# Performance work log

Hardware: AMD Instinct MI355X
Metric: run time of the kernel (lower is better)

Reference implementation:

```python
import jax, jax.numpy as jnp
import numpy as np

LN_EPS = 1e-5

def _layernorm(x):
    # LayerNorm over last dim, no affine (elementwise_affine=False)
    mu = jnp.mean(x, axis=-1, keepdims=True)
    var = jnp.var(x, axis=-1, keepdims=True)
    return (x - mu) * jax.lax.rsqrt(var + LN_EPS)

def setup_inputs() -> dict:
    key = jax.random.key(0)
    k1, k2, k3 = jax.random.split(key, 3)
    B, L, D = 2, 4096, 1024
    x = jax.random.normal(k1, (B, L, D), dtype=jnp.float32)
    W_qkv = jax.random.normal(k2, (3 * D, D), dtype=jnp.float32) * 0.02
    W_o = jax.random.normal(k3, (D, D), dtype=jnp.float32) * 0.02
    log_gamma = jnp.zeros((16,), dtype=jnp.float32)
    return {"x": x, "W_qkv": W_qkv, "W_o": W_o, "log_gamma": log_gamma}

def reference(x, W_qkv, W_o, log_gamma):
    B, L, D = x.shape
    H = log_gamma.shape[0]
    dk = D // H
    qkv = (x @ W_qkv.T).reshape(B, L, 3, H, dk)
    q, k, v = qkv[:, :, 0], qkv[:, :, 1], qkv[:, :, 2]  # [B,L,H,dk]
    k = _layernorm(k)
    gamma = jax.nn.sigmoid(log_gamma).reshape(1, H, 1, 1)  # per-head scalar decay
    # time-major for scan: [L,B,H,dk]
    qT = jnp.transpose(q, (1, 0, 2, 3))
    kT = jnp.transpose(k, (1, 0, 2, 3))
    vT = jnp.transpose(v, (1, 0, 2, 3))

    def step(S, qkv_t):
        q_t, k_t, v_t = qkv_t  # each [B,H,dk]
        # S(t) = gamma*S(t-1) + v_t (x) k_t ; shape [B,H,dk(d),dk(e)]
        S = gamma * S + v_t[..., :, None] * k_t[..., None, :]
        y_t = jnp.einsum('bhde,bhe->bhd', S, q_t)
        return S, y_t

    S0 = jnp.zeros((B, H, dk, dk), dtype=x.dtype)
    _, ys = jax.lax.scan(step, S0, (qT, kT, vT))  # ys: [L,B,H,dk]
    y = jnp.transpose(ys, (1, 0, 2, 3)).reshape(B, L, D)
    return y @ W_o.T
```

## Files before the change

### kernel.cpp

```cpp
#include <hip/hip_runtime.h>
#include <cstddef>

#define NB 2
#define NL 4096
#define ND 1024
#define NH 16
#define DKH 64
#define CK 64
#define NCH (NL / CK)
#define NM (NB * NL)
#define KD 1024

typedef __attribute__((ext_vector_type(8))) short bf16x8;
typedef __attribute__((ext_vector_type(4))) float f32x4;

__device__ __forceinline__ float dsigmoid(float x) { return 1.0f / (1.0f + __expf(-x)); }
__device__ __forceinline__ float bf2f(unsigned short u) { return __uint_as_float((unsigned)u << 16); }
__device__ __forceinline__ unsigned short f2bf(float f) {
    unsigned u = __float_as_uint(f);
    u = (u + 0x7fffu + ((u >> 16) & 1u)) >> 16;
    return (unsigned short)u;
}
__device__ __forceinline__ int swz(int row, int col) { return row * 64 + (col ^ ((row & 7) << 3)); }

__device__ __forceinline__ void gload16(const void* g, void* l) {
    __builtin_amdgcn_global_load_lds(
        (const __attribute__((address_space(1))) unsigned int*)g,
        (__attribute__((address_space(3))) unsigned int*)l, 16, 0, 0);
}

__global__ __launch_bounds__(256)
void k_cast_all(const float* __restrict__ x, const float* __restrict__ Wq,
                const float* __restrict__ Wo, unsigned short* __restrict__ xb,
                unsigned short* __restrict__ Wqb, unsigned short* __restrict__ Wob)
{
    const int N1 = NB * NL * ND / 4;
    const int N2 = 3 * ND * ND / 4;
    const int N3 = ND * ND / 4;
    const int total = N1 + N2 + N3;
    int i = blockIdx.x * 256 + threadIdx.x;
    const int stride = gridDim.x * 256;
    for (; i < total; i += stride) {
        const float4* src;
        ushort4* dst;
        int j;
        if (i < N1)            { src = (const float4*)x;  dst = (ushort4*)xb;  j = i; }
        else if (i < N1 + N2)  { src = (const float4*)Wq; dst = (ushort4*)Wqb; j = i - N1; }
        else                   { src = (const float4*)Wo; dst = (ushort4*)Wob; j = i - N1 - N2; }
        float4 v = src[j];
        ushort4 o;
        o.x = f2bf(v.x); o.y = f2bf(v.y); o.z = f2bf(v.z); o.w = f2bf(v.w);
        dst[j] = o;
    }
}

__global__ __launch_bounds__(256)
void k_gemm_qkv_bf16(const unsigned short* __restrict__ A, const unsigned short* __restrict__ Bm,
                     unsigned short* __restrict__ Qb, unsigned short* __restrict__ Kb,
                     unsigned short* __restrict__ Vb)
{
    __shared__ short As[128 * 64];
    __shared__ short Bs[128 * 64];
    const int tid = threadIdx.x;
    const int w = tid >> 6, lane = tid & 63;
    const int wr = w >> 1, wc = w & 1;
    const int lr = lane & 15, lk = lane >> 4;

    const int nbx = gridDim.x;
    const int nwg = nbx * gridDim.y;
    const int bid = blockIdx.y * nbx + blockIdx.x;
    const int sb  = (bid & 7) * (nwg >> 3) + (bid >> 3);
    const int row0 = (sb / nbx) * 128, col0 = (sb % nbx) * 128;

    const int srow = tid >> 3;
    const int schk = (tid & 7) ^ (srow & 7);
    const unsigned short* gA = A + (size_t)(row0 + srow) * KD + schk * 8;
    const unsigned short* gB = Bm + (size_t)(col0 + srow) * KD + schk * 8;
    short* lA = As + (w * 8) * 64;
    short* lB = Bs + (w * 8) * 64;

    f32x4 acc[4][4];
#pragma unroll
    for (int m = 0; m < 4; ++m)
#pragma unroll
        for (int n = 0; n < 4; ++n) acc[m][n] = (f32x4){0.f, 0.f, 0.f, 0.f};

    int arow[4], brow[4];
#pragma unroll
    for (int m = 0; m < 4; ++m) arow[m] = (wr * 64 + m * 16 + lr) * 64;
#pragma unroll
    for (int n = 0; n < 4; ++n) brow[n] = (wc * 64 + n * 16 + lr) * 64;
    const int xr = lr & 7;
    const int coff0 = ((0 * 4 + lk) ^ xr) * 8;
    const int coff1 = ((1 * 4 + lk) ^ xr) * 8;

    for (int k0 = 0; k0 < KD; k0 += 64) {
#pragma unroll
        for (int i = 0; i < 4; ++i) gload16(gA + (size_t)(i * 32) * KD + k0, lA + i * 2048);
#pragma unroll
        for (int i = 0; i < 4; ++i) gload16(gB + (size_t)(i * 32) * KD + k0, lB + i * 2048);
        __syncthreads();
#pragma unroll
        for (int kk = 0; kk < 2; ++kk) {
            const int co = kk ? coff1 : coff0;
            bf16x8 a[4], b[4];
#pragma unroll
            for (int m = 0; m < 4; ++m) a[m] = *(const bf16x8*)(As + arow[m] + co);
#pragma unroll
            for (int n = 0; n < 4; ++n) b[n] = *(const bf16x8*)(Bs + brow[n] + co);
#pragma unroll
            for (int m = 0; m < 4; ++m)
#pragma unroll
                for (int n = 0; n < 4; ++n)
                    acc[m][n] = __builtin_amdgcn_mfma_f32_16x16x32_bf16(a[m], b[n], acc[m][n], 0, 0, 0);
        }
        __syncthreads();
    }

#pragma unroll
    for (int m = 0; m < 4; ++m) {
        const int mrow0 = row0 + wr * 64 + m * 16 + lk * 4;
#pragma unroll
        for (int n = 0; n < 4; ++n) {
            const int gcol = col0 + wc * 64 + n * 16 + lr;
            const int three = gcol >> 10;
            const int h = (gcol >> 6) & (NH - 1);
            const int d = gcol & (DKH - 1);
            unsigned short* dst = (three == 0) ? Qb : ((three == 1) ? Kb : Vb);
#pragma unroll
            for (int j = 0; j < 4; ++j) {
                const int mr = mrow0 + j;
                const int b = mr >> 12;
                const int t = mr & (NL - 1);
                dst[(((size_t)b * NH + h) * NL + t) * DKH + d] = f2bf(acc[m][n][j]);
            }
        }
    }
}

__global__ __launch_bounds__(256)
void k_gemm_out_bf16(const unsigned short* __restrict__ A, const unsigned short* __restrict__ Bm,
                     float* __restrict__ C)
{
    __shared__ short As[128 * 64];
    __shared__ short Bs[128 * 64];
    const int tid = threadIdx.x;
    const int w = tid >> 6, lane = tid & 63;
    const int wr = w >> 1, wc = w & 1;
    const int lr = lane & 15, lk = lane >> 4;

    const int nbx = gridDim.x;
    const int nwg = nbx * gridDim.y;
    const int bid = blockIdx.y * nbx + blockIdx.x;
    const int sb  = (bid & 7) * (nwg >> 3) + (bid >> 3);
    const int row0 = (sb / nbx) * 128, col0 = (sb % nbx) * 128;

    const int srow = tid >> 3;
    const int schk = (tid & 7) ^ (srow & 7);
    const unsigned short* gA = A + (size_t)(row0 + srow) * KD + schk * 8;
    const unsigned short* gB = Bm + (size_t)(col0 + srow) * KD + schk * 8;
    short* lA = As + (w * 8) * 64;
    short* lB = Bs + (w * 8) * 64;

    f32x4 acc[4][4];
#pragma unroll
    for (int m = 0; m < 4; ++m)
#pragma unroll
        for (int n = 0; n < 4; ++n) acc[m][n] = (f32x4){0.f, 0.f, 0.f, 0.f};

    int arow[4], brow[4];
#pragma unroll
    for (int m = 0; m < 4; ++m) arow[m] = (wr * 64 + m * 16 + lr) * 64;
#pragma unroll
    for (int n = 0; n < 4; ++n) brow[n] = (wc * 64 + n * 16 + lr) * 64;
    const int xr = lr & 7;
    const int coff0 = ((0 * 4 + lk) ^ xr) * 8;
    const int coff1 = ((1 * 4 + lk) ^ xr) * 8;

    for (int k0 = 0; k0 < KD; k0 += 64) {
#pragma unroll
        for (int i = 0; i < 4; ++i) gload16(gA + (size_t)(i * 32) * KD + k0, lA + i * 2048);
#pragma unroll
        for (int i = 0; i < 4; ++i) gload16(gB + (size_t)(i * 32) * KD + k0, lB + i * 2048);
        __syncthreads();
#pragma unroll
        for (int kk = 0; kk < 2; ++kk) {
            const int co = kk ? coff1 : coff0;
            bf16x8 a[4], b[4];
#pragma unroll
            for (int m = 0; m < 4; ++m) a[m] = *(const bf16x8*)(As + arow[m] + co);
#pragma unroll
            for (int n = 0; n < 4; ++n) b[n] = *(const bf16x8*)(Bs + brow[n] + co);
#pragma unroll
            for (int m = 0; m < 4; ++m)
#pragma unroll
                for (int n = 0; n < 4; ++n)
                    acc[m][n] = __builtin_amdgcn_mfma_f32_16x16x32_bf16(a[m], b[n], acc[m][n], 0, 0, 0);
        }
        __syncthreads();
    }

#pragma unroll
    for (int m = 0; m < 4; ++m) {
        const int mrow0 = row0 + wr * 64 + m * 16 + lk * 4;
#pragma unroll
        for (int n = 0; n < 4; ++n) {
            const int gcol = col0 + wc * 64 + n * 16 + lr;
#pragma unroll
            for (int j = 0; j < 4; ++j)
                C[(size_t)(mrow0 + j) * ND + gcol] = acc[m][n][j];
        }
    }
}

__global__ __launch_bounds__(256)
void k_chunk_state(const unsigned short* __restrict__ Kb, const unsigned short* __restrict__ Vb,
                   const float* __restrict__ lg, unsigned short* __restrict__ SL)
{
    __shared__ unsigned short Kt[64 * 64];
    __shared__ unsigned short Vt[64 * 64];
    __shared__ float red[64][8];
    const int blk = blockIdx.x;
    const int c   = blk & (NCH - 1);
    const int bh  = blk >> 6;
    const int h   = bh & (NH - 1);
    const float gamma = dsigmoid(lg[h]);
    const float l2g = log2f(gamma);
    const int tid = threadIdx.x;
    const unsigned short* Kc = Kb + ((size_t)bh * NL + c * CK) * DKH;
    const unsigned short* Vc = Vb + ((size_t)bh * NL + c * CK) * DKH;

    const int r  = tid & 63;
    const int w4 = tid >> 6;
    const int c0 = w4 * 8;
    bf16x8 k8a = *(const bf16x8*)(Kc + (size_t)r * DKH + c0);
    bf16x8 k8b = *(const bf16x8*)(Kc + (size_t)r * DKH + c0 + 32);
    bf16x8 v8a = *(const bf16x8*)(Vc + (size_t)r * DKH + c0);
    bf16x8 v8b = *(const bf16x8*)(Vc + (size_t)r * DKH + c0 + 32);
    float sum = 0.f, sq = 0.f;
#pragma unroll
    for (int j = 0; j < 8; ++j) {
        float xa = bf2f((unsigned short)k8a[j]); sum += xa; sq += xa * xa;
        float xb = bf2f((unsigned short)k8b[j]); sum += xb; sq += xb * xb;
    }
    red[r][w4] = sum; red[r][w4 + 4] = sq;
    __syncthreads();
    float s  = red[r][0] + red[r][1] + red[r][2] + red[r][3];
    float qq = red[r][4] + red[r][5] + red[r][6] + red[r][7];
    float mu = s * (1.0f / 64.0f);
    float rstd = rsqrtf(qq * (1.0f / 64.0f) - mu * mu + 1e-5f);
    float wgt = exp2f((float)(CK - 1 - r) * l2g);
#pragma unroll
    for (int j = 0; j < 8; ++j) {
        Kt[swz(c0 + j, r)]      = f2bf((bf2f((unsigned short)k8a[j]) - mu) * rstd);
        Kt[swz(c0 + 32 + j, r)] = f2bf((bf2f((unsigned short)k8b[j]) - mu) * rstd);
        Vt[swz(c0 + j, r)]      = f2bf(bf2f((unsigned short)v8a[j]) * wgt);
        Vt[swz(c0 + 32 + j, r)] = f2bf(bf2f((unsigned short)v8b[j]) * wgt);
    }
    __syncthreads();

    const int w = tid >> 6, lane = tid & 63;
    const int wr = w >> 1, wc = w & 1;
    const int lr = lane & 15, lk = lane >> 4;
    f32x4 acc[2][2];
#pragma unroll
    for (int m = 0; m < 2; ++m)
#pragma unroll
        for (int n = 0; n < 2; ++n) acc[m][n] = (f32x4){0.f, 0.f, 0.f, 0.f};
#pragma unroll
    for (int kk = 0; kk < 2; ++kk) {
        const int so = kk * 32 + lk * 8;
        bf16x8 a[2], b[2];
#pragma unroll
        for (int m = 0; m < 2; ++m) a[m] = *(const bf16x8*)&Vt[swz(wr * 32 + m * 16 + lr, so)];
#pragma unroll
        for (int n = 0; n < 2; ++n) b[n] = *(const bf16x8*)&Kt[swz(wc * 32 + n * 16 + lr, so)];
#pragma unroll
        for (int m = 0; m < 2; ++m)
#pragma unroll
            for (int n = 0; n < 2; ++n)
                acc[m][n] = __builtin_amdgcn_mfma_f32_16x16x32_bf16(a[m], b[n], acc[m][n], 0, 0, 0);
    }

    unsigned short* out = SL + (size_t)blk * (DKH * DKH);
#pragma unroll
    for (int m = 0; m < 2; ++m)
#pragma unroll
        for (int n = 0; n < 2; ++n)
#pragma unroll
            for (int j = 0; j < 4; ++j) {
                int d = wr * 32 + m * 16 + lk * 4 + j;
                int e = wc * 32 + n * 16 + lr;
                out[d * DKH + e] = f2bf(acc[m][n][j]);
            }
}

__global__ __launch_bounds__(64)
void k_scan(const unsigned short* __restrict__ SL, const float* __restrict__ lg,
            unsigned short* __restrict__ SS)
{
    const int bh = blockIdx.x;
    const int qt = blockIdx.y;
    const int h  = bh & (NH - 1);
    const float gamma = dsigmoid(lg[h]);
    const float dc = __powf(gamma, (float)CK);
    const size_t base = (size_t)bh * NCH * (DKH * DKH) + qt * 256 + threadIdx.x * 4;
    float s0 = 0.f, s1 = 0.f, s2 = 0.f, s3 = 0.f;
    for (int c = 0; c < NCH; ++c) {
        const size_t off = base + (size_t)c * (DKH * DKH);
        ushort4 l = *(const ushort4*)(SL + off);
        ushort4 o;
        o.x = f2bf(s0); o.y = f2bf(s1); o.z = f2bf(s2); o.w = f2bf(s3);
        *(ushort4*)(SS + off) = o;
        s0 = s0 * dc + bf2f(l.x); s1 = s1 * dc + bf2f(l.y);
        s2 = s2 * dc + bf2f(l.z); s3 = s3 * dc + bf2f(l.w);
    }
}

__global__ __launch_bounds__(256)
void k_chunk_out(const unsigned short* __restrict__ Qb, const unsigned short* __restrict__ Kb,
                 const unsigned short* __restrict__ Vb, const unsigned short* __restrict__ SS,
                 const float* __restrict__ lg, unsigned short* __restrict__ Y)
{
    __shared__ unsigned short Qs[64 * 64];
    __shared__ unsigned short Ks[64 * 64];
    __shared__ unsigned short Vt[64 * 64];
    __shared__ unsigned short Ss[64 * 64];
    __shared__ unsigned short Ps[64 * 64];
    __shared__ float red[64][8];
    const int blk = blockIdx.x;
    const int c   = blk & (NCH - 1);
    const int bh  = blk >> 6;
    const int h   = bh & (NH - 1);
    const int b   = bh >> 4;
    const float gamma = dsigmoid(lg[h]);
    const float l2g = log2f(gamma);
    const int tid = threadIdx.x;
    const unsigned short* Qc = Qb + ((size_t)bh * NL + c * CK) * DKH;
    const unsigned short* Kc = Kb + ((size_t)bh * NL + c * CK) * DKH;
    const unsigned short* Vc = Vb + ((size_t)bh * NL + c * CK) * DKH;
    const unsigned short* Sc = SS + (size_t)blk * (DKH * DKH);

    const int r  = tid & 63;
    const int w4 = tid >> 6;
    const int c0 = w4 * 8;
    bf16x8 q8a = *(const bf16x8*)(Qc + (size_t)r * DKH + c0);
    bf16x8 q8b = *(const bf16x8*)(Qc + (size_t)r * DKH + c0 + 32);
    bf16x8 k8a = *(const bf16x8*)(Kc + (size_t)r * DKH + c0);
    bf16x8 k8b = *(const bf16x8*)(Kc + (size_t)r * DKH + c0 + 32);
    bf16x8 v8a = *(const bf16x8*)(Vc + (size_t)r * DKH + c0);
    bf16x8 v8b = *(const bf16x8*)(Vc + (size_t)r * DKH + c0 + 32);
    bf16x8 s8a = *(const bf16x8*)(Sc + (size_t)r * DKH + c0);
    bf16x8 s8b = *(const bf16x8*)(Sc + (size_t)r * DKH + c0 + 32);
    float sum = 0.f, sq = 0.f;
#pragma unroll
    for (int j = 0; j < 8; ++j) {
        float xa = bf2f((unsigned short)k8a[j]); sum += xa; sq += xa * xa;
        float xb = bf2f((unsigned short)k8b[j]); sum += xb; sq += xb * xb;
    }
    red[r][w4] = sum; red[r][w4 + 4] = sq;
    __syncthreads();
    float sm = red[r][0] + red[r][1] + red[r][2] + red[r][3];
    float qq = red[r][4] + red[r][5] + red[r][6] + red[r][7];
    float mu = sm * (1.0f / 64.0f);
    float rstd = rsqrtf(qq * (1.0f / 64.0f) - mu * mu + 1e-5f);
    *(bf16x8*)&Qs[swz(r, c0)]      = q8a;
    *(bf16x8*)&Qs[swz(r, c0 + 32)] = q8b;
    *(bf16x8*)&Ss[swz(r, c0)]      = s8a;
    *(bf16x8*)&Ss[swz(r, c0 + 32)] = s8b;
#pragma unroll
    for (int j = 0; j < 8; ++j) {
        Ks[swz(r, c0 + j)]      = f2bf((bf2f((unsigned short)k8a[j]) - mu) * rstd);
        Ks[swz(r, c0 + 32 + j)] = f2bf((bf2f((unsigned short)k8b[j]) - mu) * rstd);
        Vt[swz(c0 + j, r)]      = (unsigned short)v8a[j];
        Vt[swz(c0 + 32 + j, r)] = (unsigned short)v8b[j];
    }
    __syncthreads();

    const int w = tid >> 6, lane = tid & 63;
    const int wr = w >> 1, wc = w & 1;
    const int lr = lane & 15, lk = lane >> 4;

    f32x4 accp[2][2];
#pragma unroll
    for (int m = 0; m < 2; ++m)
#pragma unroll
        for (int n = 0; n < 2; ++n) accp[m][n] = (f32x4){0.f, 0.f, 0.f, 0.f};
#pragma unroll
    for (int kk = 0; kk < 2; ++kk) {
        const int eo = kk * 32 + lk * 8;
        bf16x8 a[2], bfr[2];
#pragma unroll
        for (int m = 0; m < 2; ++m) a[m]   = *(const bf16x8*)&Qs[swz(wr * 32 + m * 16 + lr, eo)];
#pragma unroll
        for (int n = 0; n < 2; ++n) bfr[n] = *(const bf16x8*)&Ks[swz(wc * 32 + n * 16 + lr, eo)];
#pragma unroll
        for (int m = 0; m < 2; ++m)
#pragma unroll
            for (int n = 0; n < 2; ++n)
                accp[m][n] = __builtin_amdgcn_mfma_f32_16x16x32_bf16(a[m], bfr[n], accp[m][n], 0, 0, 0);
    }
#pragma unroll
    for (int m = 0; m < 2; ++m)
#pragma unroll
        for (int n = 0; n < 2; ++n)
#pragma unroll
            for (int j = 0; j < 4; ++j) {
                int t = wr * 32 + m * 16 + lk * 4 + j;
                int s = wc * 32 + n * 16 + lr;
                int dt = t - s;
                float v = (dt >= 0) ? accp[m][n][j] * exp2f((float)dt * l2g) : 0.0f;
                Ps[swz(t, s)] = f2bf(v);
            }
    __syncthreads();

    f32x4 accy[2][2], accz[2][2];
#pragma unroll
    for (int m = 0; m < 2; ++m)
#pragma unroll
        for (int n = 0; n < 2; ++n) {
            accy[m][n] = (f32x4){0.f, 0.f, 0.f, 0.f};
            accz[m][n] = (f32x4){0.f, 0.f, 0.f, 0.f};
        }
#pragma unroll
    for (int kk = 0; kk < 2; ++kk) {
        const int so = kk * 32 + lk * 8;
        bf16x8 pa[2], qa[2], vb[2], sb[2];
#pragma unroll
        for (int m = 0; m < 2; ++m) {
            pa[m] = *(const bf16x8*)&Ps[swz(wr * 32 + m * 16 + lr, so)];
            qa[m] = *(const bf16x8*)&Qs[swz(wr * 32 + m * 16 + lr, so)];
        }
#pragma unroll
        for (int n = 0; n < 2; ++n) {
            vb[n] = *(const bf16x8*)&Vt[swz(wc * 32 + n * 16 + lr, so)];
            sb[n] = *(const bf16x8*)&Ss[swz(wc * 32 + n * 16 + lr, so)];
        }
#pragma unroll
        for (int m = 0; m < 2; ++m)
#pragma unroll
            for (int n = 0; n < 2; ++n) {
                accy[m][n] = __builtin_amdgcn_mfma_f32_16x16x32_bf16(pa[m], vb[n], accy[m][n], 0, 0, 0);
                accz[m][n] = __builtin_amdgcn_mfma_f32_16x16x32_bf16(qa[m], sb[n], accz[m][n], 0, 0, 0);
            }
    }
    __syncthreads();

#pragma unroll
    for (int m = 0; m < 2; ++m)
#pragma unroll
        for (int n = 0; n < 2; ++n)
#pragma unroll
            for (int j = 0; j < 4; ++j) {
                int t = wr * 32 + m * 16 + lk * 4 + j;
                int d = wc * 32 + n * 16 + lr;
                float g = exp2f((float)(t + 1) * l2g);
                Ps[swz(t, d)] = f2bf(accy[m][n][j] + g * accz[m][n][j]);
            }
    __syncthreads();

#pragma unroll
    for (int i = 0; i < 2; ++i) {
        int f  = tid + i * 256;
        int rr = f >> 3;
        int ch = f & 7;
        bf16x8 val = *(const bf16x8*)&Ps[swz(rr, ch * 8)];
        unsigned short* p = Y + ((size_t)(b * NL + c * CK + rr)) * ND + h * DKH + ch * 8;
        *(bf16x8*)p = val;
    }
}

extern "C" void kernel_launch(void* const* d_in, const int* in_sizes, int n_in,
                              void* d_out, int out_size, void* d_ws, size_t ws_size,
                              hipStream_t stream)
{
    (void)in_sizes; (void)n_in; (void)out_size; (void)ws_size;
    const float* x  = (const float*)d_in[0];
    const float* Wq = (const float*)d_in[1];
    const float* Wo = (const float*)d_in[2];
    const float* lg = (const float*)d_in[3];
    float* out = (float*)d_out;

    const size_t SZ = (size_t)NB * NH * NL * DKH;
    unsigned short* xb  = (unsigned short*)d_ws;
    unsigned short* Wqb = xb + SZ;
    unsigned short* Wob = Wqb + (size_t)3 * ND * ND;
    unsigned short* Qb  = Wob + (size_t)ND * ND;
    unsigned short* Kb  = Qb + SZ;
    unsigned short* Vb  = Kb + SZ;
    unsigned short* SL  = Vb + SZ;
    unsigned short* SS  = SL + SZ;
    unsigned short* Ybb = SS + SZ;

    k_cast_all<<<2048, 256, 0, stream>>>(x, Wq, Wo, xb, Wqb, Wob);
    k_gemm_qkv_bf16<<<dim3(3 * ND / 128, NM / 128), 256, 0, stream>>>(xb, Wqb, Qb, Kb, Vb);
    k_chunk_state<<<dim3(NB * NH * NCH), 256, 0, stream>>>(Kb, Vb, lg, SL);
    k_scan<<<dim3(NB * NH, 16), 64, 0, stream>>>(SL, lg, SS);
    k_chunk_out<<<dim3(NB * NH * NCH), 256, 0, stream>>>(Qb, Kb, Vb, SS, lg, Ybb);
    k_gemm_out_bf16<<<dim3(ND / 128, NM / 128), 256, 0, stream>>>(Ybb, Wob, out);
}
```

Before: 135.3 us.

## Group four chunks per block and carry intra-group state in registers

State computation and the inter-chunk scan now work on groups of four 64-token chunks. Each block of the output kernel keeps the running state in MFMA accumulators and updates it chunk by chunk, so the scan covers 16 groups instead of 64 chunks and less state is written to and read from global memory. The price is a quarter as many blocks (512) in the state and output kernels, which lowers parallelism on the GPU, plus extra MFMA work and LDS traffic per chunk inside the output kernel. Next-chunk loads are double-buffered in registers to hide global latency.

```diff
diff --git a/kernel.cpp b/kernel.cpp
--- a/kernel.cpp
+++ b/kernel.cpp
@@ -8,6 +8,7 @@
 #define DKH 64
 #define CK 64
 #define NCH (NL / CK)
+#define NG 16
 #define NM (NB * NL)
 #define KD 1024
 
@@ -214,75 +215,99 @@
 }
 
 __global__ __launch_bounds__(256)
-void k_chunk_state(const unsigned short* __restrict__ Kb, const unsigned short* __restrict__ Vb,
-                   const float* __restrict__ lg, unsigned short* __restrict__ SL)
+void k_group_state(const unsigned short* __restrict__ Kb, const unsigned short* __restrict__ Vb,
+                   const float* __restrict__ lg, unsigned short* __restrict__ GL)
 {
     __shared__ unsigned short Kt[64 * 64];
     __shared__ unsigned short Vt[64 * 64];
     __shared__ float red[64][8];
     const int blk = blockIdx.x;
-    const int c   = blk & (NCH - 1);
-    const int bh  = blk >> 6;
+    const int g   = blk & (NG - 1);
+    const int bh  = blk >> 4;
     const int h   = bh & (NH - 1);
     const float gamma = dsigmoid(lg[h]);
-    const float l2g = log2f(gamma);
+    const float l2g  = log2f(gamma);
+    const float dc64 = exp2f(64.0f * l2g);
     const int tid = threadIdx.x;
-    const unsigned short* Kc = Kb + ((size_t)bh * NL + c * CK) * DKH;
-    const unsigned short* Vc = Vb + ((size_t)bh * NL + c * CK) * DKH;
-
     const int r  = tid & 63;
     const int w4 = tid >> 6;
     const int c0 = w4 * 8;
-    bf16x8 k8a = *(const bf16x8*)(Kc + (size_t)r * DKH + c0);
-    bf16x8 k8b = *(const bf16x8*)(Kc + (size_t)r * DKH + c0 + 32);
-    bf16x8 v8a = *(const bf16x8*)(Vc + (size_t)r * DKH + c0);
-    bf16x8 v8b = *(const bf16x8*)(Vc + (size_t)r * DKH + c0 + 32);
-    float sum = 0.f, sq = 0.f;
-#pragma unroll
-    for (int j = 0; j < 8; ++j) {
-        float xa = bf2f((unsigned short)k8a[j]); sum += xa; sq += xa * xa;
-        float xb = bf2f((unsigned short)k8b[j]); sum += xb; sq += xb * xb;
-    }
-    red[r][w4] = sum; red[r][w4 + 4] = sq;
-    __syncthreads();
-    float s  = red[r][0] + red[r][1] + red[r][2] + red[r][3];
-    float qq = red[r][4] + red[r][5] + red[r][6] + red[r][7];
-    float mu = s * (1.0f / 64.0f);
-    float rstd = rsqrtf(qq * (1.0f / 64.0f) - mu * mu + 1e-5f);
-    float wgt = exp2f((float)(CK - 1 - r) * l2g);
-#pragma unroll
-    for (int j = 0; j < 8; ++j) {
-        Kt[swz(c0 + j, r)]      = f2bf((bf2f((unsigned short)k8a[j]) - mu) * rstd);
-        Kt[swz(c0 + 32 + j, r)] = f2bf((bf2f((unsigned short)k8b[j]) - mu) * rstd);
-        Vt[swz(c0 + j, r)]      = f2bf(bf2f((unsigned short)v8a[j]) * wgt);
-        Vt[swz(c0 + 32 + j, r)] = f2bf(bf2f((unsigned short)v8b[j]) * wgt);
-    }
-    __syncthreads();
-
     const int w = tid >> 6, lane = tid & 63;
     const int wr = w >> 1, wc = w & 1;
     const int lr = lane & 15, lk = lane >> 4;
+
     f32x4 acc[2][2];
 #pragma unroll
     for (int m = 0; m < 2; ++m)
 #pragma unroll
         for (int n = 0; n < 2; ++n) acc[m][n] = (f32x4){0.f, 0.f, 0.f, 0.f};
-#pragma unroll
-    for (int kk = 0; kk < 2; ++kk) {
-        const int so = kk * 32 + lk * 8;
-        bf16x8 a[2], b[2];
-#pragma unroll
-        for (int m = 0; m < 2; ++m) a[m] = *(const bf16x8*)&Vt[swz(wr * 32 + m * 16 + lr, so)];
-#pragma unroll
-        for (int n = 0; n < 2; ++n) b[n] = *(const bf16x8*)&Kt[swz(wc * 32 + n * 16 + lr, so)];
-#pragma unroll
-        for (int m = 0; m < 2; ++m)
-#pragma unroll
-            for (int n = 0; n < 2; ++n)
-                acc[m][n] = __builtin_amdgcn_mfma_f32_16x16x32_bf16(a[m], b[n], acc[m][n], 0, 0, 0);
-    }
-
-    unsigned short* out = SL + (size_t)blk * (DKH * DKH);
+
+    bf16x8 k8[2][2], v8[2][2];
+    {
+        const unsigned short* Kc = Kb + ((size_t)bh * NL + (g * 4) * CK) * DKH;
+        const unsigned short* Vc = Vb + ((size_t)bh * NL + (g * 4) * CK) * DKH;
+        k8[0][0] = *(const bf16x8*)(Kc + (size_t)r * DKH + c0);
+        k8[0][1] = *(const bf16x8*)(Kc + (size_t)r * DKH + c0 + 32);
+        v8[0][0] = *(const bf16x8*)(Vc + (size_t)r * DKH + c0);
+        v8[0][1] = *(const bf16x8*)(Vc + (size_t)r * DKH + c0 + 32);
+    }
+
+#pragma unroll
+    for (int ci = 0; ci < 4; ++ci) {
+        const int cb = ci & 1;
+        float sum = 0.f, sq = 0.f;
+#pragma unroll
+        for (int j = 0; j < 8; ++j) {
+            float xa = bf2f((unsigned short)k8[cb][0][j]); sum += xa; sq += xa * xa;
+            float xb = bf2f((unsigned short)k8[cb][1][j]); sum += xb; sq += xb * xb;
+        }
+        red[r][w4] = sum; red[r][w4 + 4] = sq;
+        __syncthreads();
+        float sm = red[r][0] + red[r][1] + red[r][2] + red[r][3];
+        float qq = red[r][4] + red[r][5] + red[r][6] + red[r][7];
+        float mu = sm * (1.0f / 64.0f);
+        float rstd = rsqrtf(qq * (1.0f / 64.0f) - mu * mu + 1e-5f);
+        float wgt = exp2f((float)(CK - 1 - r) * l2g);
+#pragma unroll
+        for (int j = 0; j < 8; ++j) {
+            Kt[swz(c0 + j, r)]      = f2bf((bf2f((unsigned short)k8[cb][0][j]) - mu) * rstd * wgt);
+            Kt[swz(c0 + 32 + j, r)] = f2bf((bf2f((unsigned short)k8[cb][1][j]) - mu) * rstd * wgt);
+            Vt[swz(c0 + j, r)]      = (unsigned short)v8[cb][0][j];
+            Vt[swz(c0 + 32 + j, r)] = (unsigned short)v8[cb][1][j];
+        }
+        if (ci < 3) {
+            const int c = g * 4 + ci + 1;
+            const unsigned short* Kc = Kb + ((size_t)bh * NL + c * CK) * DKH;
+            const unsigned short* Vc = Vb + ((size_t)bh * NL + c * CK) * DKH;
+            k8[cb ^ 1][0] = *(const bf16x8*)(Kc + (size_t)r * DKH + c0);
+            k8[cb ^ 1][1] = *(const bf16x8*)(Kc + (size_t)r * DKH + c0 + 32);
+            v8[cb ^ 1][0] = *(const bf16x8*)(Vc + (size_t)r * DKH + c0);
+            v8[cb ^ 1][1] = *(const bf16x8*)(Vc + (size_t)r * DKH + c0 + 32);
+        }
+        __syncthreads();
+        if (ci > 0) {
+#pragma unroll
+            for (int m = 0; m < 2; ++m)
+#pragma unroll
+                for (int n = 0; n < 2; ++n) acc[m][n] = acc[m][n] * dc64;
+        }
+#pragma unroll
+        for (int kk = 0; kk < 2; ++kk) {
+            const int so = kk * 32 + lk * 8;
+            bf16x8 a[2], b[2];
+#pragma unroll
+            for (int m = 0; m < 2; ++m) a[m] = *(const bf16x8*)&Vt[swz(wr * 32 + m * 16 + lr, so)];
+#pragma unroll
+            for (int n = 0; n < 2; ++n) b[n] = *(const bf16x8*)&Kt[swz(wc * 32 + n * 16 + lr, so)];
+#pragma unroll
+            for (int m = 0; m < 2; ++m)
+#pragma unroll
+                for (int n = 0; n < 2; ++n)
+                    acc[m][n] = __builtin_amdgcn_mfma_f32_16x16x32_bf16(a[m], b[n], acc[m][n], 0, 0, 0);
+        }
+    }
+
+    unsigned short* out = GL + (size_t)blk * (DKH * DKH);
 #pragma unroll
     for (int m = 0; m < 2; ++m)
 #pragma unroll
@@ -296,177 +321,224 @@
 }
 
 __global__ __launch_bounds__(64)
-void k_scan(const unsigned short* __restrict__ SL, const float* __restrict__ lg,
-            unsigned short* __restrict__ SS)
+void k_scan16(const unsigned short* __restrict__ GL, const float* __restrict__ lg,
+              unsigned short* __restrict__ GS)
 {
     const int bh = blockIdx.x;
     const int qt = blockIdx.y;
     const int h  = bh & (NH - 1);
     const float gamma = dsigmoid(lg[h]);
-    const float dc = __powf(gamma, (float)CK);
-    const size_t base = (size_t)bh * NCH * (DKH * DKH) + qt * 256 + threadIdx.x * 4;
+    const float dc = exp2f(256.0f * log2f(gamma));
+    const size_t base = (size_t)bh * NG * (DKH * DKH) + qt * 256 + threadIdx.x * 4;
     float s0 = 0.f, s1 = 0.f, s2 = 0.f, s3 = 0.f;
-    for (int c = 0; c < NCH; ++c) {
-        const size_t off = base + (size_t)c * (DKH * DKH);
-        ushort4 l = *(const ushort4*)(SL + off);
+    for (int g = 0; g < NG; ++g) {
+        const size_t off = base + (size_t)g * (DKH * DKH);
+        ushort4 l = *(const ushort4*)(GL + off);
         ushort4 o;
         o.x = f2bf(s0); o.y = f2bf(s1); o.z = f2bf(s2); o.w = f2bf(s3);
-        *(ushort4*)(SS + off) = o;
+        *(ushort4*)(GS + off) = o;
         s0 = s0 * dc + bf2f(l.x); s1 = s1 * dc + bf2f(l.y);
         s2 = s2 * dc + bf2f(l.z); s3 = s3 * dc + bf2f(l.w);
     }
 }
 
 __global__ __launch_bounds__(256)
-void k_chunk_out(const unsigned short* __restrict__ Qb, const unsigned short* __restrict__ Kb,
-                 const unsigned short* __restrict__ Vb, const unsigned short* __restrict__ SS,
-                 const float* __restrict__ lg, unsigned short* __restrict__ Y)
+void k_chunk_out4(const unsigned short* __restrict__ Qb, const unsigned short* __restrict__ Kb,
+                  const unsigned short* __restrict__ Vb, const unsigned short* __restrict__ GS,
+                  const float* __restrict__ lg, unsigned short* __restrict__ Y)
 {
     __shared__ unsigned short Qs[64 * 64];
     __shared__ unsigned short Ks[64 * 64];
+    __shared__ unsigned short Kwt[64 * 64];
     __shared__ unsigned short Vt[64 * 64];
-    __shared__ unsigned short Ss[64 * 64];
     __shared__ unsigned short Ps[64 * 64];
+    __shared__ unsigned short Sbf[64 * 64];
     __shared__ float red[64][8];
     const int blk = blockIdx.x;
-    const int c   = blk & (NCH - 1);
-    const int bh  = blk >> 6;
+    const int g   = blk & (NG - 1);
+    const int bh  = blk >> 4;
     const int h   = bh & (NH - 1);
     const int b   = bh >> 4;
     const float gamma = dsigmoid(lg[h]);
-    const float l2g = log2f(gamma);
+    const float l2g  = log2f(gamma);
+    const float dc64 = exp2f(64.0f * l2g);
     const int tid = threadIdx.x;
-    const unsigned short* Qc = Qb + ((size_t)bh * NL + c * CK) * DKH;
-    const unsigned short* Kc = Kb + ((size_t)bh * NL + c * CK) * DKH;
-    const unsigned short* Vc = Vb + ((size_t)bh * NL + c * CK) * DKH;
-    const unsigned short* Sc = SS + (size_t)blk * (DKH * DKH);
-
     const int r  = tid & 63;
     const int w4 = tid >> 6;
     const int c0 = w4 * 8;
-    bf16x8 q8a = *(const bf16x8*)(Qc + (size_t)r * DKH + c0);
-    bf16x8 q8b = *(const bf16x8*)(Qc + (size_t)r * DKH + c0 + 32);
-    bf16x8 k8a = *(const bf16x8*)(Kc + (size_t)r * DKH + c0);
-    bf16x8 k8b = *(const bf16x8*)(Kc + (size_t)r * DKH + c0 + 32);
-    bf16x8 v8a = *(const bf16x8*)(Vc + (size_t)r * DKH + c0);
-    bf16x8 v8b = *(const bf16x8*)(Vc + (size_t)r * DKH + c0 + 32);
-    bf16x8 s8a = *(const bf16x8*)(Sc + (size_t)r * DKH + c0);
-    bf16x8 s8b = *(const bf16x8*)(Sc + (size_t)r * DKH + c0 + 32);
-    float sum = 0.f, sq = 0.f;
-#pragma unroll
-    for (int j = 0; j < 8; ++j) {
-        float xa = bf2f((unsigned short)k8a[j]); sum += xa; sq += xa * xa;
-        float xb = bf2f((unsigned short)k8b[j]); sum += xb; sq += xb * xb;
-    }
-    red[r][w4] = sum; red[r][w4 + 4] = sq;
-    __syncthreads();
-    float sm = red[r][0] + red[r][1] + red[r][2] + red[r][3];
-    float qq = red[r][4] + red[r][5] + red[r][6] + red[r][7];
-    float mu = sm * (1.0f / 64.0f);
-    float rstd = rsqrtf(qq * (1.0f / 64.0f) - mu * mu + 1e-5f);
-    *(bf16x8*)&Qs[swz(r, c0)]      = q8a;
-    *(bf16x8*)&Qs[swz(r, c0 + 32)] = q8b;
-    *(bf16x8*)&Ss[swz(r, c0)]      = s8a;
-    *(bf16x8*)&Ss[swz(r, c0 + 32)] = s8b;
-#pragma unroll
-    for (int j = 0; j < 8; ++j) {
-        Ks[swz(r, c0 + j)]      = f2bf((bf2f((unsigned short)k8a[j]) - mu) * rstd);
-        Ks[swz(r, c0 + 32 + j)] = f2bf((bf2f((unsigned short)k8b[j]) - mu) * rstd);
-        Vt[swz(c0 + j, r)]      = (unsigned short)v8a[j];
-        Vt[swz(c0 + 32 + j, r)] = (unsigned short)v8b[j];
-    }
-    __syncthreads();
-
     const int w = tid >> 6, lane = tid & 63;
     const int wr = w >> 1, wc = w & 1;
     const int lr = lane & 15, lk = lane >> 4;
 
-    f32x4 accp[2][2];
+    {
+        const unsigned short* Gp = GS + (size_t)blk * (DKH * DKH);
+        *(bf16x8*)&Sbf[swz(r, c0)]      = *(const bf16x8*)(Gp + (size_t)r * DKH + c0);
+        *(bf16x8*)&Sbf[swz(r, c0 + 32)] = *(const bf16x8*)(Gp + (size_t)r * DKH + c0 + 32);
+    }
+    __syncthreads();
+    f32x4 S_acc[2][2];
 #pragma unroll
     for (int m = 0; m < 2; ++m)
 #pragma unroll
-        for (int n = 0; n < 2; ++n) accp[m][n] = (f32x4){0.f, 0.f, 0.f, 0.f};
-#pragma unroll
-    for (int kk = 0; kk < 2; ++kk) {
-        const int eo = kk * 32 + lk * 8;
-        bf16x8 a[2], bfr[2];
-#pragma unroll
-        for (int m = 0; m < 2; ++m) a[m]   = *(const bf16x8*)&Qs[swz(wr * 32 + m * 16 + lr, eo)];
-#pragma unroll
-        for (int n = 0; n < 2; ++n) bfr[n] = *(const bf16x8*)&Ks[swz(wc * 32 + n * 16 + lr, eo)];
+        for (int n = 0; n < 2; ++n)
+#pragma unroll
+            for (int j = 0; j < 4; ++j)
+                S_acc[m][n][j] = bf2f(Sbf[swz(wr * 32 + m * 16 + lk * 4 + j, wc * 32 + n * 16 + lr)]);
+
+    bf16x8 q8[2][2], k8[2][2], v8[2][2];
+    {
+        const size_t rowb = ((size_t)bh * NL + (g * 4) * CK + r) * DKH;
+        q8[0][0] = *(const bf16x8*)(Qb + rowb + c0);
+        q8[0][1] = *(const bf16x8*)(Qb + rowb + c0 + 32);
+        k8[0][0] = *(const bf16x8*)(Kb + rowb + c0);
+        k8[0][1] = *(const bf16x8*)(Kb + rowb + c0 + 32);
+        v8[0][0] = *(const bf16x8*)(Vb + rowb + c0);
+        v8[0][1] = *(const bf16x8*)(Vb + rowb + c0 + 32);
+    }
+
+#pragma unroll
+    for (int ci = 0; ci < 4; ++ci) {
+        const int cb = ci & 1;
+        const int c  = g * 4 + ci;
+        float sum = 0.f, sq = 0.f;
+#pragma unroll
+        for (int j = 0; j < 8; ++j) {
+            float xa = bf2f((unsigned short)k8[cb][0][j]); sum += xa; sq += xa * xa;
+            float xb = bf2f((unsigned short)k8[cb][1][j]); sum += xb; sq += xb * xb;
+        }
+        red[r][w4] = sum; red[r][w4 + 4] = sq;
+        __syncthreads();
+        float sm = red[r][0] + red[r][1] + red[r][2] + red[r][3];
+        float qq = red[r][4] + red[r][5] + red[r][6] + red[r][7];
+        float mu = sm * (1.0f / 64.0f);
+        float rstd = rsqrtf(qq * (1.0f / 64.0f) - mu * mu + 1e-5f);
+        float wgt = exp2f((float)(CK - 1 - r) * l2g);
+        *(bf16x8*)&Qs[swz(r, c0)]      = q8[cb][0];
+        *(bf16x8*)&Qs[swz(r, c0 + 32)] = q8[cb][1];
+#pragma unroll
+        for (int j = 0; j < 8; ++j) {
+            float ka = (bf2f((unsigned short)k8[cb][0][j]) - mu) * rstd;
+            float kb_ = (bf2f((unsigned short)k8[cb][1][j]) - mu) * rstd;
+            Ks[swz(r, c0 + j)]       = f2bf(ka);
+            Ks[swz(r, c0 + 32 + j)]  = f2bf(kb_);
+            Kwt[swz(c0 + j, r)]      = f2bf(ka * wgt);
+            Kwt[swz(c0 + 32 + j, r)] = f2bf(kb_ * wgt);
+            Vt[swz(c0 + j, r)]       = (unsigned short)v8[cb][0][j];
+            Vt[swz(c0 + 32 + j, r)]  = (unsigned short)v8[cb][1][j];
+        }
 #pragma unroll
         for (int m = 0; m < 2; ++m)
 #pragma unroll
             for (int n = 0; n < 2; ++n)
-                accp[m][n] = __builtin_amdgcn_mfma_f32_16x16x32_bf16(a[m], bfr[n], accp[m][n], 0, 0, 0);
-    }
-#pragma unroll
-    for (int m = 0; m < 2; ++m)
-#pragma unroll
-        for (int n = 0; n < 2; ++n)
-#pragma unroll
-            for (int j = 0; j < 4; ++j) {
-                int t = wr * 32 + m * 16 + lk * 4 + j;
-                int s = wc * 32 + n * 16 + lr;
-                int dt = t - s;
-                float v = (dt >= 0) ? accp[m][n][j] * exp2f((float)dt * l2g) : 0.0f;
-                Ps[swz(t, s)] = f2bf(v);
+#pragma unroll
+                for (int j = 0; j < 4; ++j)
+                    Sbf[swz(wr * 32 + m * 16 + lk * 4 + j, wc * 32 + n * 16 + lr)] =
+                        f2bf(S_acc[m][n][j]);
+        __syncthreads();
+
+        f32x4 accp[2][2];
+#pragma unroll
+        for (int m = 0; m < 2; ++m)
+#pragma unroll
+            for (int n = 0; n < 2; ++n) accp[m][n] = (f32x4){0.f, 0.f, 0.f, 0.f};
+#pragma unroll
+        for (int kk = 0; kk < 2; ++kk) {
+            const int eo = kk * 32 + lk * 8;
+            bf16x8 a[2], bfr[2];
+#pragma unroll
+            for (int m = 0; m < 2; ++m) a[m]   = *(const bf16x8*)&Qs[swz(wr * 32 + m * 16 + lr, eo)];
+#pragma unroll
+            for (int n = 0; n < 2; ++n) bfr[n] = *(const bf16x8*)&Ks[swz(wc * 32 + n * 16 + lr, eo)];
+#pragma unroll
+            for (int m = 0; m < 2; ++m)
+#pragma unroll
+                for (int n = 0; n < 2; ++n)
+                    accp[m][n] = __builtin_amdgcn_mfma_f32_16x16x32_bf16(a[m], bfr[n], accp[m][n], 0, 0, 0);
+        }
+#pragma unroll
+        for (int m = 0; m < 2; ++m)
+#pragma unroll
+            for (int n = 0; n < 2; ++n)
+#pragma unroll
+                for (int j = 0; j < 4; ++j) {
+                    int t = wr * 32 + m * 16 + lk * 4 + j;
+                    int s = wc * 32 + n * 16 + lr;
+                    int dt = t - s;
+                    float v = (dt >= 0) ? accp[m][n][j] * exp2f((float)dt * l2g) : 0.0f;
+                    Ps[swz(t, s)] = f2bf(v);
+                }
+        if (ci < 3) {
+            const size_t rowb = ((size_t)bh * NL + (c + 1) * CK + r) * DKH;
+            q8[cb ^ 1][0] = *(const bf16x8*)(Qb + rowb + c0);
+            q8[cb ^ 1][1] = *(const bf16x8*)(Qb + rowb + c0 + 32);
+            k8[cb ^ 1][0] = *(const bf16x8*)(Kb + rowb + c0);
+            k8[cb ^ 1][1] = *(const bf16x8*)(Kb + rowb + c0 + 32);
+            v8[cb ^ 1][0] = *(const bf16x8*)(Vb + rowb + c0);
+            v8[cb ^ 1][1] = *(const bf16x8*)(Vb + rowb + c0 + 32);
+        }
+        __syncthreads();
+
+#pragma unroll
+        for (int m = 0; m < 2; ++m)
+#pragma unroll
+            for (int n = 0; n < 2; ++n) S_acc[m][n] = S_acc[m][n] * dc64;
+        f32x4 accy[2][2], accz[2][2];
+#pragma unroll
+        for (int m = 0; m < 2; ++m)
+#pragma unroll
+            for (int n = 0; n < 2; ++n) {
+                accy[m][n] = (f32x4){0.f, 0.f, 0.f, 0.f};
+                accz[m][n] = (f32x4){0.f, 0.f, 0.f, 0.f};
             }
-    __syncthreads();
-
-    f32x4 accy[2][2], accz[2][2];
-#pragma unroll
-    for (int m = 0; m < 2; ++m)
-#pragma unroll
-        for (int n = 0; n < 2; ++n) {
-            accy[m][n] = (f32x4){0.f, 0.f, 0.f, 0.f};
-            accz[m][n] = (f32x4){0.f, 0.f, 0.f, 0.f};
-        }
-#pragma unroll
-    for (int kk = 0; kk < 2; ++kk) {
-        const int so = kk * 32 + lk * 8;
-        bf16x8 pa[2], qa[2], vb[2], sb[2];
-#pragma unroll
-        for (int m = 0; m < 2; ++m) {
-            pa[m] = *(const bf16x8*)&Ps[swz(wr * 32 + m * 16 + lr, so)];
-            qa[m] = *(const bf16x8*)&Qs[swz(wr * 32 + m * 16 + lr, so)];
-        }
-#pragma unroll
-        for (int n = 0; n < 2; ++n) {
-            vb[n] = *(const bf16x8*)&Vt[swz(wc * 32 + n * 16 + lr, so)];
-            sb[n] = *(const bf16x8*)&Ss[swz(wc * 32 + n * 16 + lr, so)];
-        }
+#pragma unroll
+        for (int kk = 0; kk < 2; ++kk) {
+            const int so = kk * 32 + lk * 8;
+            bf16x8 pa[2], qa[2], va[2], vb[2], sb[2], kb2[2];
+#pragma unroll
+            for (int m = 0; m < 2; ++m) {
+                pa[m] = *(const bf16x8*)&Ps[swz(wr * 32 + m * 16 + lr, so)];
+                qa[m] = *(const bf16x8*)&Qs[swz(wr * 32 + m * 16 + lr, so)];
+                va[m] = *(const bf16x8*)&Vt[swz(wr * 32 + m * 16 + lr, so)];
+            }
+#pragma unroll
+            for (int n = 0; n < 2; ++n) {
+                vb[n]  = *(const bf16x8*)&Vt[swz(wc * 32 + n * 16 + lr, so)];
+                sb[n]  = *(const bf16x8*)&Sbf[swz(wc * 32 + n * 16 + lr, so)];
+                kb2[n] = *(const bf16x8*)&Kwt[swz(wc * 32 + n * 16 + lr, so)];
+            }
+#pragma unroll
+            for (int m = 0; m < 2; ++m)
+#pragma unroll
+                for (int n = 0; n < 2; ++n) {
+                    accy[m][n]  = __builtin_amdgcn_mfma_f32_16x16x32_bf16(pa[m], vb[n],  accy[m][n], 0, 0, 0);
+                    accz[m][n]  = __builtin_amdgcn_mfma_f32_16x16x32_bf16(qa[m], sb[n],  accz[m][n], 0, 0, 0);
+                    S_acc[m][n] = __builtin_amdgcn_mfma_f32_16x16x32_bf16(va[m], kb2[n], S_acc[m][n], 0, 0, 0);
+                }
+        }
+        __syncthreads();
+
 #pragma unroll
         for (int m = 0; m < 2; ++m)
 #pragma unroll
-            for (int n = 0; n < 2; ++n) {
-                accy[m][n] = __builtin_amdgcn_mfma_f32_16x16x32_bf16(pa[m], vb[n], accy[m][n], 0, 0, 0);
-                accz[m][n] = __builtin_amdgcn_mfma_f32_16x16x32_bf16(qa[m], sb[n], accz[m][n], 0, 0, 0);
-            }
-    }
-    __syncthreads();
-
-#pragma unroll
-    for (int m = 0; m < 2; ++m)
-#pragma unroll
-        for (int n = 0; n < 2; ++n)
-#pragma unroll
-            for (int j = 0; j < 4; ++j) {
-                int t = wr * 32 + m * 16 + lk * 4 + j;
-                int d = wc * 32 + n * 16 + lr;
-                float g = exp2f((float)(t + 1) * l2g);
-                Ps[swz(t, d)] = f2bf(accy[m][n][j] + g * accz[m][n][j]);
-            }
-    __syncthreads();
-
-#pragma unroll
-    for (int i = 0; i < 2; ++i) {
-        int f  = tid + i * 256;
-        int rr = f >> 3;
-        int ch = f & 7;
-        bf16x8 val = *(const bf16x8*)&Ps[swz(rr, ch * 8)];
-        unsigned short* p = Y + ((size_t)(b * NL + c * CK + rr)) * ND + h * DKH + ch * 8;
-        *(bf16x8*)p = val;
+            for (int n = 0; n < 2; ++n)
+#pragma unroll
+                for (int j = 0; j < 4; ++j) {
+                    int t = wr * 32 + m * 16 + lk * 4 + j;
+                    int d = wc * 32 + n * 16 + lr;
+                    float ge = exp2f((float)(t + 1) * l2g);
+                    Ps[swz(t, d)] = f2bf(accy[m][n][j] + ge * accz[m][n][j]);
+                }
+        __syncthreads();
+
+#pragma unroll
+        for (int i = 0; i < 2; ++i) {
+            int f  = tid + i * 256;
+            int rr = f >> 3;
+            int ch = f & 7;
+            bf16x8 val = *(const bf16x8*)&Ps[swz(rr, ch * 8)];
+            unsigned short* p = Y + ((size_t)(b * NL + c * CK + rr)) * ND + h * DKH + ch * 8;
+            *(bf16x8*)p = val;
+        }
     }
 }
 
@@ -481,21 +553,22 @@
     const float* lg = (const float*)d_in[3];
     float* out = (float*)d_out;
 
-    const size_t SZ = (size_t)NB * NH * NL * DKH;
+    const size_t SZ  = (size_t)NB * NH * NL * DKH;
+    const size_t GSZ = (size_t)NB * NH * NG * DKH * DKH;
     unsigned short* xb  = (unsigned short*)d_ws;
     unsigned short* Wqb = xb + SZ;
     unsigned short* Wob = Wqb + (size_t)3 * ND * ND;
     unsigned short* Qb  = Wob + (size_t)ND * ND;
     unsigned short* Kb  = Qb + SZ;
     unsigned short* Vb  = Kb + SZ;
-    unsigned short* SL  = Vb + SZ;
-    unsigned short* SS  = SL + SZ;
-    unsigned short* Ybb = SS + SZ;
+    unsigned short* GL  = Vb + SZ;
+    unsigned short* GS  = GL + GSZ;
+    unsigned short* Ybb = GS + GSZ;
 
     k_cast_all<<<2048, 256, 0, stream>>>(x, Wq, Wo, xb, Wqb, Wob);
     k_gemm_qkv_bf16<<<dim3(3 * ND / 128, NM / 128), 256, 0, stream>>>(xb, Wqb, Qb, Kb, Vb);
-    k_chunk_state<<<dim3(NB * NH * NCH), 256, 0, stream>>>(Kb, Vb, lg, SL);
-    k_scan<<<dim3(NB * NH, 16), 64, 0, stream>>>(SL, lg, SS);
-    k_chunk_out<<<dim3(NB * NH * NCH), 256, 0, stream>>>(Qb, Kb, Vb, SS, lg, Ybb);
+    k_group_state<<<dim3(NB * NH * NG), 256, 0, stream>>>(Kb, Vb, lg, GL);
+    k_scan16<<<dim3(NB * NH, 16), 64, 0, stream>>>(GL, lg, GS);
+    k_chunk_out4<<<dim3(NB * NH * NG), 256, 0, stream>>>(Qb, Kb, Vb, GS, lg, Ybb);
     k_gemm_out_bf16<<<dim3(ND / 128, NM / 128), 256, 0, stream>>>(Ybb, Wob, out);
 }
```

After: 136.0 us. Within noise of the previous version (+0.5%).

## Fuse K layernorm into QKV GEMM epilogue and widen cast kernel stores

Applied to the files above, without the earlier changes.

The per-head layernorm of K moves into the QKV GEMM epilogue, using wave shuffles across the 64 columns each wave holds per head. This removes the duplicated LN reduction, shared-memory reduction array and extra barrier from both chunk kernels. In k_chunk_state the decay weight now scales K instead of V, which is mathematically equivalent. The cast kernel also handles 8 elements per thread with 16-byte stores. The cost is extra epilogue work in the GEMM blocks that produce K, and K is now rounded to bf16 after normalisation rather than before.

```diff
diff --git a/kernel.cpp b/kernel.cpp
--- a/kernel.cpp
+++ b/kernel.cpp
@@ -34,22 +34,26 @@
                 const float* __restrict__ Wo, unsigned short* __restrict__ xb,
                 unsigned short* __restrict__ Wqb, unsigned short* __restrict__ Wob)
 {
-    const int N1 = NB * NL * ND / 4;
-    const int N2 = 3 * ND * ND / 4;
-    const int N3 = ND * ND / 4;
+    const int N1 = NB * NL * ND / 8;
+    const int N2 = 3 * ND * ND / 8;
+    const int N3 = ND * ND / 8;
     const int total = N1 + N2 + N3;
     int i = blockIdx.x * 256 + threadIdx.x;
     const int stride = gridDim.x * 256;
     for (; i < total; i += stride) {
         const float4* src;
-        ushort4* dst;
+        bf16x8* dst;
         int j;
-        if (i < N1)            { src = (const float4*)x;  dst = (ushort4*)xb;  j = i; }
-        else if (i < N1 + N2)  { src = (const float4*)Wq; dst = (ushort4*)Wqb; j = i - N1; }
-        else                   { src = (const float4*)Wo; dst = (ushort4*)Wob; j = i - N1 - N2; }
-        float4 v = src[j];
-        ushort4 o;
-        o.x = f2bf(v.x); o.y = f2bf(v.y); o.z = f2bf(v.z); o.w = f2bf(v.w);
+        if (i < N1)            { src = (const float4*)x;  dst = (bf16x8*)xb;  j = i; }
+        else if (i < N1 + N2)  { src = (const float4*)Wq; dst = (bf16x8*)Wqb; j = i - N1; }
+        else                   { src = (const float4*)Wo; dst = (bf16x8*)Wob; j = i - N1 - N2; }
+        float4 a = src[2 * j];
+        float4 b = src[2 * j + 1];
+        bf16x8 o;
+        o[0] = (short)f2bf(a.x); o[1] = (short)f2bf(a.y);
+        o[2] = (short)f2bf(a.z); o[3] = (short)f2bf(a.w);
+        o[4] = (short)f2bf(b.x); o[5] = (short)f2bf(b.y);
+        o[6] = (short)f2bf(b.z); o[7] = (short)f2bf(b.w);
         dst[j] = o;
     }
 }
@@ -117,6 +121,25 @@
         __syncthreads();
     }
 
+    if ((col0 >> 10) == 1) {
+#pragma unroll
+        for (int m = 0; m < 4; ++m)
+#pragma unroll
+            for (int j = 0; j < 4; ++j) {
+                float s = 0.f, q = 0.f;
+#pragma unroll
+                for (int n = 0; n < 4; ++n) { float v = acc[m][n][j]; s += v; q += v * v; }
+                s += __shfl_xor(s, 1); q += __shfl_xor(q, 1);
+                s += __shfl_xor(s, 2); q += __shfl_xor(q, 2);
+                s += __shfl_xor(s, 4); q += __shfl_xor(q, 4);
+                s += __shfl_xor(s, 8); q += __shfl_xor(q, 8);
+                float mu = s * (1.0f / 64.0f);
+                float rstd = rsqrtf(q * (1.0f / 64.0f) - mu * mu + 1e-5f);
+#pragma unroll
+                for (int n = 0; n < 4; ++n) acc[m][n][j] = (acc[m][n][j] - mu) * rstd;
+            }
+    }
+
 #pragma unroll
     for (int m = 0; m < 4; ++m) {
         const int mrow0 = row0 + wr * 64 + m * 16 + lk * 4;
@@ -219,7 +242,6 @@
 {
     __shared__ unsigned short Kt[64 * 64];
     __shared__ unsigned short Vt[64 * 64];
-    __shared__ float red[64][8];
     const int blk = blockIdx.x;
     const int c   = blk & (NCH - 1);
     const int bh  = blk >> 6;
@@ -237,25 +259,13 @@
     bf16x8 k8b = *(const bf16x8*)(Kc + (size_t)r * DKH + c0 + 32);
     bf16x8 v8a = *(const bf16x8*)(Vc + (size_t)r * DKH + c0);
     bf16x8 v8b = *(const bf16x8*)(Vc + (size_t)r * DKH + c0 + 32);
-    float sum = 0.f, sq = 0.f;
+    float wgt = exp2f((float)(CK - 1 - r) * l2g);
 #pragma unroll
     for (int j = 0; j < 8; ++j) {
-        float xa = bf2f((unsigned short)k8a[j]); sum += xa; sq += xa * xa;
-        float xb = bf2f((unsigned short)k8b[j]); sum += xb; sq += xb * xb;
-    }
-    red[r][w4] = sum; red[r][w4 + 4] = sq;
-    __syncthreads();
-    float s  = red[r][0] + red[r][1] + red[r][2] + red[r][3];
-    float qq = red[r][4] + red[r][5] + red[r][6] + red[r][7];
-    float mu = s * (1.0f / 64.0f);
-    float rstd = rsqrtf(qq * (1.0f / 64.0f) - mu * mu + 1e-5f);
-    float wgt = exp2f((float)(CK - 1 - r) * l2g);
-#pragma unroll
-    for (int j = 0; j < 8; ++j) {
-        Kt[swz(c0 + j, r)]      = f2bf((bf2f((unsigned short)k8a[j]) - mu) * rstd);
-        Kt[swz(c0 + 32 + j, r)] = f2bf((bf2f((unsigned short)k8b[j]) - mu) * rstd);
-        Vt[swz(c0 + j, r)]      = f2bf(bf2f((unsigned short)v8a[j]) * wgt);
-        Vt[swz(c0 + 32 + j, r)] = f2bf(bf2f((unsigned short)v8b[j]) * wgt);
+        Kt[swz(c0 + j, r)]      = f2bf(bf2f((unsigned short)k8a[j]) * wgt);
+        Kt[swz(c0 + 32 + j, r)] = f2bf(bf2f((unsigned short)k8b[j]) * wgt);
+        Vt[swz(c0 + j, r)]      = (unsigned short)v8a[j];
+        Vt[swz(c0 + 32 + j, r)] = (unsigned short)v8b[j];
     }
     __syncthreads();
 
@@ -327,7 +337,6 @@
     __shared__ unsigned short Vt[64 * 64];
     __shared__ unsigned short Ss[64 * 64];
     __shared__ unsigned short Ps[64 * 64];
-    __shared__ float red[64][8];
     const int blk = blockIdx.x;
     const int c   = blk & (NCH - 1);
     const int bh  = blk >> 6;
@@ -352,26 +361,14 @@
     bf16x8 v8b = *(const bf16x8*)(Vc + (size_t)r * DKH + c0 + 32);
     bf16x8 s8a = *(const bf16x8*)(Sc + (size_t)r * DKH + c0);
     bf16x8 s8b = *(const bf16x8*)(Sc + (size_t)r * DKH + c0 + 32);
-    float sum = 0.f, sq = 0.f;
-#pragma unroll
-    for (int j = 0; j < 8; ++j) {
-        float xa = bf2f((unsigned short)k8a[j]); sum += xa; sq += xa * xa;
-        float xb = bf2f((unsigned short)k8b[j]); sum += xb; sq += xb * xb;
-    }
-    red[r][w4] = sum; red[r][w4 + 4] = sq;
-    __syncthreads();
-    float sm = red[r][0] + red[r][1] + red[r][2] + red[r][3];
-    float qq = red[r][4] + red[r][5] + red[r][6] + red[r][7];
-    float mu = sm * (1.0f / 64.0f);
-    float rstd = rsqrtf(qq * (1.0f / 64.0f) - mu * mu + 1e-5f);
     *(bf16x8*)&Qs[swz(r, c0)]      = q8a;
     *(bf16x8*)&Qs[swz(r, c0 + 32)] = q8b;
+    *(bf16x8*)&Ks[swz(r, c0)]      = k8a;
+    *(bf16x8*)&Ks[swz(r, c0 + 32)] = k8b;
     *(bf16x8*)&Ss[swz(r, c0)]      = s8a;
     *(bf16x8*)&Ss[swz(r, c0 + 32)] = s8b;
 #pragma unroll
     for (int j = 0; j < 8; ++j) {
-        Ks[swz(r, c0 + j)]      = f2bf((bf2f((unsigned short)k8a[j]) - mu) * rstd);
-        Ks[swz(r, c0 + 32 + j)] = f2bf((bf2f((unsigned short)k8b[j]) - mu) * rstd);
         Vt[swz(c0 + j, r)]      = (unsigned short)v8a[j];
         Vt[swz(c0 + 32 + j, r)] = (unsigned short)v8b[j];
     }
```

Result: slower. 140.2 us (+3.7%).
